# Kernel tuning notes

Measured on AMD Instinct MI355X. Metric: run time of the kernel, lower is better.

## Reference

```python
import jax, jax.numpy as jnp
import numpy as np
import math

DIM = 2048      # model dim
NH = 16         # query heads
NKV = 8         # kv heads
NREP = NH // NKV
HD = DIM // (2 * NH)   # 64: per-half head dim (q/k per head = 2*HD)
HIDDEN = 5632   # multiple_of*ceil(int(8*DIM/3)/multiple_of), multiple_of=256
EPS = 1e-5
LAMBDA = 0.8 - 0.6 * math.exp(-0.3 * 0)  # depth=0 -> 0.2
ROPE_THETA = 10000.0


def rmsnorm(x, w):
    xf = x.astype(jnp.float32)
    return (w * (xf * jax.lax.rsqrt(jnp.mean(xf * xf, axis=-1, keepdims=True) + EPS))).astype(x.dtype)


def rope(x, cos, sin):
    # x: (B, L, H, 2*HD) with interleaved (even, odd) complex pairs; cos/sin: (L, HD)
    xe, xo = x[..., 0::2], x[..., 1::2]
    c = cos[None, :, None, :]
    s = sin[None, :, None, :]
    re = xe * c - xo * s
    ro = xe * s + xo * c
    return jnp.stack([re, ro], axis=-1).reshape(x.shape)


def setup_inputs() -> dict:
    key = jax.random.key(0)
    ks = jax.random.split(key, 12)
    B, L = 1, 2048
    x = jax.random.normal(ks[0], (B, L, DIM), dtype=jnp.float32)
    # RoPE tables for per-head q/k dim 2*HD -> HD frequencies
    inv_freq = 1.0 / (ROPE_THETA ** (np.arange(0, 2 * HD, 2, dtype=np.float32) / (2 * HD)))
    t = np.arange(L, dtype=np.float32)
    ang = np.outer(t, inv_freq)  # (L, HD)
    freqs_cos = jnp.asarray(np.cos(ang), dtype=jnp.float32)
    freqs_sin = jnp.asarray(np.sin(ang), dtype=jnp.float32)
    sc = 0.02
    return {
        'x': x,
        'freqs_cos': freqs_cos,
        'freqs_sin': freqs_sin,
        'attn_norm_w': jnp.ones((DIM,), jnp.float32),
        'wq': jax.random.normal(ks[1], (DIM, DIM), jnp.float32) * sc,
        'wk': jax.random.normal(ks[2], (DIM, DIM // NREP), jnp.float32) * sc,
        'wv': jax.random.normal(ks[3], (DIM, DIM // NREP), jnp.float32) * sc,
        'wo': jax.random.normal(ks[4], (DIM, DIM), jnp.float32) * sc,
        'ffn_norm_w': jnp.ones((DIM,), jnp.float32),
        'w1': jax.random.normal(ks[5], (DIM, HIDDEN), jnp.float32) * sc,
        'w2': jax.random.normal(ks[6], (HIDDEN, DIM), jnp.float32) * sc,
        'w3': jax.random.normal(ks[7], (DIM, HIDDEN), jnp.float32) * sc,
    }


def reference(x, freqs_cos, freqs_sin, attn_norm_w, wq, wk, wv, wo, ffn_norm_w, w1, w2, w3):
    B, L, _ = x.shape
    # ---- attention branch ----
    h = rmsnorm(x, attn_norm_w)
    q = (h @ wq).reshape(B, L, NH, 2 * HD)
    k = (h @ wk).reshape(B, L, NKV, 2 * HD)
    v = (h @ wv).reshape(B, L, NKV, 2 * HD)
    q = rope(q, freqs_cos, freqs_sin)
    k = rope(k, freqs_cos, freqs_sin)
    k = jnp.repeat(k, NREP, axis=2)  # GQA expansion -> (B, L, NH, 2*HD)
    v = jnp.repeat(v, NREP, axis=2)
    q1, q2 = q[..., :HD], q[..., HD:]
    k1, k2 = k[..., :HD], k[..., HD:]
    scale = 1.0 / math.sqrt(HD)
    sc1 = jnp.einsum('bqhd,bkhd->bhqk', q1, k1) * scale
    sc2 = jnp.einsum('bqhd,bkhd->bhqk', q2, k2) * scale
    causal = jnp.tril(jnp.ones((L, L), dtype=bool))
    neg = jnp.float32(-jnp.inf)
    a1 = jax.nn.softmax(jnp.where(causal, sc1, neg), axis=-1)
    a2 = jax.nn.softmax(jnp.where(causal, sc2, neg), axis=-1)
    attn = a1 - LAMBDA * a2  # differential attention
    out = jnp.einsum('bhqk,bkhd->bqhd', attn, v).reshape(B, L, DIM)
    h2 = x + out @ wo
    # ---- SwiGLU FFN branch ----
    f = rmsnorm(h2, ffn_norm_w)
    ffn = (jax.nn.silu(f @ w1) * (f @ w3)) @ w2
    return h2 + ffn
```

## Files before the change

### kernel.cpp

```cpp
#include <hip/hip_runtime.h>
#include <hip/hip_bf16.h>

#define DIMSZ 2048
#define LSEQ 2048
#define NHEADS 16
#define NKVH 8
#define HDIM 128
#define HHALF 64
#define EPSV 1e-5f
#define LAMB 0.2f
#define SM_SCALE 0.125f

typedef __attribute__((ext_vector_type(8))) short bf16x8;
typedef __attribute__((ext_vector_type(4))) float f32x4;
typedef __hip_bfloat16 bf16;

__device__ __forceinline__ void gload_lds16(const void* g, void* l) {
    __builtin_amdgcn_global_load_lds((const __attribute__((address_space(1))) void*)g,
                                     (__attribute__((address_space(3))) void*)l, 16, 0, 0);
}

template<typename T> __device__ __forceinline__ T cvt_out(float v);
template<> __device__ __forceinline__ float cvt_out<float>(float v) { return v; }
template<> __device__ __forceinline__ bf16  cvt_out<bf16>(float v)  { return __float2bfloat16(v); }

__global__ __launch_bounds__(256) void rmsnorm_kernel(const float* __restrict__ x,
                                                      const float* __restrict__ w,
                                                      bf16* __restrict__ out)
{
    int row = blockIdx.x;
    int t = threadIdx.x;
    const float* xr = x + (size_t)row * DIMSZ;
    float4 v0 = ((const float4*)xr)[t];
    float4 v1 = ((const float4*)xr)[t + 256];
    float s = v0.x*v0.x + v0.y*v0.y + v0.z*v0.z + v0.w*v0.w
            + v1.x*v1.x + v1.y*v1.y + v1.z*v1.z + v1.w*v1.w;
    #pragma unroll
    for (int m = 1; m < 64; m <<= 1) s += __shfl_xor(s, m, 64);
    __shared__ float red[4];
    int wid = t >> 6;
    if ((t & 63) == 0) red[wid] = s;
    __syncthreads();
    float tot = red[0] + red[1] + red[2] + red[3];
    float inv = rsqrtf(tot * (1.0f / DIMSZ) + EPSV);
    float4 w0 = ((const float4*)w)[t];
    float4 w1v = ((const float4*)w)[t + 256];
    bf16* orow = out + (size_t)row * DIMSZ;
    orow[t*4 + 0] = __float2bfloat16(v0.x*inv*w0.x);
    orow[t*4 + 1] = __float2bfloat16(v0.y*inv*w0.y);
    orow[t*4 + 2] = __float2bfloat16(v0.z*inv*w0.z);
    orow[t*4 + 3] = __float2bfloat16(v0.w*inv*w0.w);
    orow[1024 + t*4 + 0] = __float2bfloat16(v1.x*inv*w1v.x);
    orow[1024 + t*4 + 1] = __float2bfloat16(v1.y*inv*w1v.y);
    orow[1024 + t*4 + 2] = __float2bfloat16(v1.z*inv*w1v.z);
    orow[1024 + t*4 + 3] = __float2bfloat16(v1.w*inv*w1v.w);
}

__global__ __launch_bounds__(256) void tcast_kernel(const float* __restrict__ in,
                                                    bf16* __restrict__ out,
                                                    int K, int N)
{
    __shared__ float tile[32][33];
    int bx = blockIdx.x, by = blockIdx.y;
    int tx = threadIdx.x & 31, tr = threadIdx.x >> 5;
    const float* src = in + (size_t)(by*32 + tr) * N + bx*32 + tx;
    #pragma unroll
    for (int r = 0; r < 32; r += 8)
        tile[tr + r][tx] = src[(size_t)r * N];
    __syncthreads();
    bf16* dst = out + (size_t)(bx*32 + tr) * K + by*32 + tx;
    #pragma unroll
    for (int r = 0; r < 32; r += 8)
        dst[(size_t)r * K] = __float2bfloat16(tile[tx][tr + r]);
}

__global__ __launch_bounds__(256) void rope_cast_kernel(const float* __restrict__ buf,
                                                        const float* __restrict__ cosT,
                                                        const float* __restrict__ sinT,
                                                        bf16* __restrict__ out,
                                                        int log2nh)
{
    int idx = blockIdx.x * 256 + threadIdx.x;
    int j = idx & 63;
    int hl = idx >> 6;
    int l = hl >> log2nh;
    float c = cosT[l * 64 + j];
    float s = sinT[l * 64 + j];
    float2 v = ((const float2*)buf)[idx];
    __hip_bfloat162 rr;
    rr.x = __float2bfloat16(v.x * c - v.y * s);
    rr.y = __float2bfloat16(v.x * s + v.y * c);
    ((__hip_bfloat162*)out)[idx] = rr;
}

template<int EPI, typename CT>
__global__ __launch_bounds__(256) void gemm_bf16(const bf16* __restrict__ A,
                                                 const bf16* __restrict__ BT,
                                                 CT* __restrict__ C,
                                                 const float* __restrict__ R,
                                                 int M, int N, int K)
{
    constexpr int BK = 32;
    __shared__ alignas(16) bf16 As[128 * BK];
    __shared__ alignas(16) bf16 Bs[128 * BK];
    int t = threadIdx.x;
    int lane = t & 63, wid = t >> 6;
    int wr = wid >> 1, wc = wid & 1;
    int row0 = blockIdx.y * 128, col0 = blockIdx.x * 128;

    f32x4 acc[4][4];
    #pragma unroll
    for (int i = 0; i < 4; ++i)
        #pragma unroll
        for (int j = 0; j < 4; ++j)
            acc[i][j] = (f32x4){0.f, 0.f, 0.f, 0.f};

    for (int k0 = 0; k0 < K; k0 += BK) {
        __syncthreads();
        #pragma unroll
        for (int s = 0; s < 2; ++s) {
            int c = s * 256 + t;
            int row = c >> 2, kc = c & 3;
            gload_lds16(A  + (size_t)(row0 + row) * K + k0 + kc * 8, (char*)As + c * 16);
            gload_lds16(BT + (size_t)(col0 + row) * K + k0 + kc * 8, (char*)Bs + c * 16);
        }
        __syncthreads();

        bf16x8 a[4], b[4];
        int ch = lane >> 4;
        #pragma unroll
        for (int i = 0; i < 4; ++i) {
            int ra = wr * 64 + i * 16 + (lane & 15);
            int rb = wc * 64 + i * 16 + (lane & 15);
            a[i] = *(const bf16x8*)((const char*)As + ra * 64 + ch * 16);
            b[i] = *(const bf16x8*)((const char*)Bs + rb * 64 + ch * 16);
        }
        #pragma unroll
        for (int i = 0; i < 4; ++i)
            #pragma unroll
            for (int j = 0; j < 4; ++j)
                acc[i][j] = __builtin_amdgcn_mfma_f32_16x16x32_bf16(a[i], b[j], acc[i][j], 0, 0, 0);
    }

    int rl = lane >> 4;
    int cl = lane & 15;
    #pragma unroll
    for (int i = 0; i < 4; ++i) {
        #pragma unroll
        for (int j = 0; j < 4; ++j) {
            #pragma unroll
            for (int r = 0; r < 4; ++r) {
                int row = row0 + wr * 64 + i * 16 + rl * 4 + r;
                int col = col0 + wc * 64 + j * 16 + cl;
                size_t idx = (size_t)row * N + col;
                float v = acc[i][j][r];
                if (EPI == 1) v += R[idx];
                else if (EPI == 2) { float uv = R[idx]; v = (uv / (1.0f + __expf(-uv))) * v; }
                C[idx] = cvt_out<CT>(v);
            }
        }
    }
}

__global__ __launch_bounds__(256) void attn_mfma_kernel(const bf16* __restrict__ Qb,
                                                        const bf16* __restrict__ Kb,
                                                        const bf16* __restrict__ Vt,
                                                        bf16* __restrict__ O)
{
    int qb = (int)gridDim.x - 1 - (int)blockIdx.x;
    int h = blockIdx.y;
    int kvh = h >> 1;
    int t = threadIdx.x;
    int lane = t & 63, w = t >> 6;
    int lr = lane & 15;
    int lk = lane >> 4;

    __shared__ alignas(16) bf16 Ksm[64 * 128];
    __shared__ alignas(16) bf16 Vsm[128 * 64];
    __shared__ alignas(16) bf16 Psm[2][64 * 64];

    bf16x8 qf[4];
    {
        const char* qrow = (const char*)Qb + ((size_t)(qb * 64 + w * 16 + lr) * (NHEADS * HDIM) + h * HDIM) * 2;
        #pragma unroll
        for (int s = 0; s < 4; ++s)
            qf[s] = *(const bf16x8*)(qrow + (s * 32 + lk * 8) * 2);
    }

    f32x4 o1[8], o2[8];
    #pragma unroll
    for (int d = 0; d < 8; ++d) { o1[d] = (f32x4){0.f,0.f,0.f,0.f}; o2[d] = (f32x4){0.f,0.f,0.f,0.f}; }
    float m1[4], l1[4], m2[4], l2[4];
    #pragma unroll
    for (int r = 0; r < 4; ++r) { m1[r] = -1e30f; m2[r] = -1e30f; l1[r] = 0.f; l2[r] = 0.f; }

    int nt = qb + 1;
    for (int it = 0; it < nt; ++it) {
        int k0 = it * 64;
        bf16x8 kreg[4], vreg[4];
        #pragma unroll
        for (int c4 = 0; c4 < 4; ++c4) {
            int c = c4 * 256 + t;
            int key = c >> 4, db = (c & 15) * 16;
            kreg[c4] = *(const bf16x8*)((const char*)Kb
                        + (size_t)(k0 + key) * (NKVH * HDIM * 2) + kvh * HDIM * 2 + db);
            int d = c >> 3, kbyte = (c & 7) * 16;
            vreg[c4] = *(const bf16x8*)((const char*)Vt
                        + ((size_t)(kvh * HDIM + d) * LSEQ + k0) * 2 + kbyte);
        }
        __syncthreads();
        #pragma unroll
        for (int c4 = 0; c4 < 4; ++c4) {
            int c = c4 * 256 + t;
            int key = c >> 4, db = (c & 15) * 16;
            *(bf16x8*)((char*)Ksm + ((key * 256 + db) ^ ((key & 7) << 4))) = kreg[c4];
            int d = c >> 3, kbyte = (c & 7) * 16;
            *(bf16x8*)((char*)Vsm + ((d * 128 + kbyte) ^ ((d & 7) << 4))) = vreg[c4];
        }
        __syncthreads();

        f32x4 s1a[4], s2a[4];
        #pragma unroll
        for (int ct = 0; ct < 4; ++ct) { s1a[ct] = (f32x4){0.f,0.f,0.f,0.f}; s2a[ct] = (f32x4){0.f,0.f,0.f,0.f}; }
        #pragma unroll
        for (int ct = 0; ct < 4; ++ct) {
            int key = ct * 16 + lr;
            int kswz = (key & 7) << 4;
            #pragma unroll
            for (int s = 0; s < 2; ++s) {
                bf16x8 kb1 = *(const bf16x8*)((const char*)Ksm + ((key * 256 + (s * 32 + lk * 8) * 2) ^ kswz));
                bf16x8 kb2 = *(const bf16x8*)((const char*)Ksm + ((key * 256 + (64 + s * 32 + lk * 8) * 2) ^ kswz));
                s1a[ct] = __builtin_amdgcn_mfma_f32_16x16x32_bf16(qf[s],     kb1, s1a[ct], 0, 0, 0);
                s2a[ct] = __builtin_amdgcn_mfma_f32_16x16x32_bf16(qf[2 + s], kb2, s2a[ct], 0, 0, 0);
            }
        }

        bool diag = (it == nt - 1);
        #pragma unroll
        for (int r = 0; r < 4; ++r) {
            int rowl = w * 16 + lk * 4 + r;
            int rg = qb * 64 + rowl;
            float v1[4], v2[4];
            #pragma unroll
            for (int ct = 0; ct < 4; ++ct) {
                v1[ct] = s1a[ct][r] * SM_SCALE;
                v2[ct] = s2a[ct][r] * SM_SCALE;
                if (diag) {
                    int cg = k0 + ct * 16 + lr;
                    if (cg > rg) { v1[ct] = -1e30f; v2[ct] = -1e30f; }
                }
            }
            float tm1 = fmaxf(fmaxf(v1[0], v1[1]), fmaxf(v1[2], v1[3]));
            float tm2 = fmaxf(fmaxf(v2[0], v2[1]), fmaxf(v2[2], v2[3]));
            #pragma unroll
            for (int msk = 1; msk < 16; msk <<= 1) {
                tm1 = fmaxf(tm1, __shfl_xor(tm1, msk, 64));
                tm2 = fmaxf(tm2, __shfl_xor(tm2, msk, 64));
            }
            float mn1 = fmaxf(m1[r], tm1), mn2 = fmaxf(m2[r], tm2);
            float ts1 = 0.f, ts2 = 0.f;
            #pragma unroll
            for (int ct = 0; ct < 4; ++ct) {
                v1[ct] = __expf(v1[ct] - mn1);
                v2[ct] = __expf(v2[ct] - mn2);
                ts1 += v1[ct]; ts2 += v2[ct];
            }
            #pragma unroll
            for (int msk = 1; msk < 16; msk <<= 1) {
                ts1 += __shfl_xor(ts1, msk, 64);
                ts2 += __shfl_xor(ts2, msk, 64);
            }
            float sc1 = __expf(m1[r] - mn1), sc2 = __expf(m2[r] - mn2);
            l1[r] = l1[r] * sc1 + ts1;
            l2[r] = l2[r] * sc2 + ts2;
            m1[r] = mn1; m2[r] = mn2;
            #pragma unroll
            for (int d = 0; d < 8; ++d) { o1[d][r] *= sc1; o2[d][r] *= sc2; }
            int pswz = ((rowl ^ (rowl >> 3)) & 7) << 4;
            #pragma unroll
            for (int ct = 0; ct < 4; ++ct) {
                int byte0 = (rowl * 128 + (ct * 16 + lr) * 2) ^ pswz;
                *(bf16*)((char*)Psm[0] + byte0) = __float2bfloat16(v1[ct]);
                *(bf16*)((char*)Psm[1] + byte0) = __float2bfloat16(v2[ct]);
            }
        }
        asm volatile("s_waitcnt lgkmcnt(0)" ::: "memory");
        __builtin_amdgcn_sched_barrier(0);

        int prow = w * 16 + lr;
        int pswz2 = ((prow ^ (prow >> 3)) & 7) << 4;
        bf16x8 p1f[2], p2f[2];
        #pragma unroll
        for (int s = 0; s < 2; ++s) {
            int pb = (prow * 128 + (s * 32 + lk * 8) * 2) ^ pswz2;
            p1f[s] = *(const bf16x8*)((const char*)Psm[0] + pb);
            p2f[s] = *(const bf16x8*)((const char*)Psm[1] + pb);
        }
        #pragma unroll
        for (int dt = 0; dt < 8; ++dt) {
            int d = dt * 16 + lr;
            int vswz = (d & 7) << 4;
            #pragma unroll
            for (int s = 0; s < 2; ++s) {
                bf16x8 vf = *(const bf16x8*)((const char*)Vsm + ((d * 128 + (s * 32 + lk * 8) * 2) ^ vswz));
                o1[dt] = __builtin_amdgcn_mfma_f32_16x16x32_bf16(p1f[s], vf, o1[dt], 0, 0, 0);
                o2[dt] = __builtin_amdgcn_mfma_f32_16x16x32_bf16(p2f[s], vf, o2[dt], 0, 0, 0);
            }
        }
    }

    #pragma unroll
    for (int r = 0; r < 4; ++r) {
        float inv1 = 1.0f / l1[r];
        float inv2 = LAMB / l2[r];
        bf16* dst = O + (size_t)(qb * 64 + w * 16 + lk * 4 + r) * DIMSZ + h * HDIM;
        #pragma unroll
        for (int dt = 0; dt < 8; ++dt)
            dst[dt * 16 + lr] = __float2bfloat16(o1[dt][r] * inv1 - o2[dt][r] * inv2);
    }
}

extern "C" void kernel_launch(void* const* d_in, const int* in_sizes, int n_in,
                              void* d_out, int out_size, void* d_ws, size_t ws_size,
                              hipStream_t stream)
{
    const float* x      = (const float*)d_in[0];
    const float* fcos   = (const float*)d_in[1];
    const float* fsin   = (const float*)d_in[2];
    const float* attn_w = (const float*)d_in[3];
    const float* wq     = (const float*)d_in[4];
    const float* wk     = (const float*)d_in[5];
    const float* wv     = (const float*)d_in[6];
    const float* wo     = (const float*)d_in[7];
    const float* ffn_w  = (const float*)d_in[8];
    const float* w1     = (const float*)d_in[9];
    const float* w2     = (const float*)d_in[10];
    const float* w3     = (const float*)d_in[11];
    float* out = (float*)d_out;
    char*  wsb = (char*)d_ws;

    bf16*  h    = (bf16*) (wsb + 0);
    float* q    = (float*)(wsb + (size_t)( 8u << 20));
    float* kb   = (float*)(wsb + (size_t)(24u << 20));
    float* vb   = (float*)(wsb + (size_t)(32u << 20));
    bf16*  q_bf = (bf16*) (wsb + 0);
    bf16*  k_bf = (bf16*) (wsb + (size_t)( 8u << 20));
    bf16*  vt   = (bf16*) (wsb + (size_t)(12u << 20));
    bf16*  att  = (bf16*) (wsb + (size_t)(40u << 20));
    float* u    = (float*)(wsb + 0);
    bf16*  f    = (bf16*) (wsb + (size_t)(48u << 20));
    bf16*  g    = (bf16*) (wsb + (size_t)(56u << 20));
    bf16*  W    = (bf16*) (wsb + (size_t)(80u << 20));

    dim3 blk(256);

    rmsnorm_kernel<<<LSEQ, blk, 0, stream>>>(x, attn_w, h);

    tcast_kernel<<<dim3(64, 64), blk, 0, stream>>>(wq, W, 2048, 2048);
    gemm_bf16<0, float><<<dim3(16, 16), blk, 0, stream>>>(h, W, q, nullptr, 2048, 2048, 2048);
    tcast_kernel<<<dim3(32, 64), blk, 0, stream>>>(wk, W, 2048, 1024);
    gemm_bf16<0, float><<<dim3(8, 16), blk, 0, stream>>>(h, W, kb, nullptr, 2048, 1024, 2048);
    tcast_kernel<<<dim3(32, 64), blk, 0, stream>>>(wv, W, 2048, 1024);
    gemm_bf16<0, float><<<dim3(8, 16), blk, 0, stream>>>(h, W, vb, nullptr, 2048, 1024, 2048);

    rope_cast_kernel<<<(LSEQ * NHEADS * 64) / 256, blk, 0, stream>>>(q, fcos, fsin, q_bf, 4);
    rope_cast_kernel<<<(LSEQ * NKVH * 64) / 256, blk, 0, stream>>>(kb, fcos, fsin, k_bf, 3);
    tcast_kernel<<<dim3(32, 64), blk, 0, stream>>>(vb, vt, 2048, 1024);

    attn_mfma_kernel<<<dim3(LSEQ / 64, NHEADS), blk, 0, stream>>>(q_bf, k_bf, vt, att);

    tcast_kernel<<<dim3(64, 64), blk, 0, stream>>>(wo, W, 2048, 2048);
    gemm_bf16<1, float><<<dim3(16, 16), blk, 0, stream>>>(att, W, out, x, 2048, 2048, 2048);

    rmsnorm_kernel<<<LSEQ, blk, 0, stream>>>(out, ffn_w, f);

    tcast_kernel<<<dim3(176, 64), blk, 0, stream>>>(w1, W, 2048, 5632);
    gemm_bf16<0, float><<<dim3(44, 16), blk, 0, stream>>>(f, W, u, nullptr, 2048, 5632, 2048);
    tcast_kernel<<<dim3(176, 64), blk, 0, stream>>>(w3, W, 2048, 5632);
    gemm_bf16<2, bf16><<<dim3(44, 16), blk, 0, stream>>>(f, W, g, u, 2048, 5632, 2048);
    tcast_kernel<<<dim3(64, 176), blk, 0, stream>>>(w2, W, 5632, 2048);
    gemm_bf16<1, float><<<dim3(16, 16), blk, 0, stream>>>(g, W, out, out, 2048, 2048, 5632);
}
```

Before: 938.0 us.

## Fuse QKV and W1/W3 GEMMs, split-K the Wo and W2 projections

Result: faster. 781.6 us (-16.7%).

```diff
diff --git a/kernel.cpp b/kernel.cpp
--- a/kernel.cpp
+++ b/kernel.cpp
@@ -18,6 +18,11 @@
 __device__ __forceinline__ void gload_lds16(const void* g, void* l) {
     __builtin_amdgcn_global_load_lds((const __attribute__((address_space(1))) void*)g,
                                      (__attribute__((address_space(3))) void*)l, 16, 0, 0);
+}
+
+__device__ __forceinline__ float bf2f(short s) {
+    unsigned u = ((unsigned)(unsigned short)s) << 16;
+    return __builtin_bit_cast(float, u);
 }
 
 template<typename T> __device__ __forceinline__ T cvt_out(float v);
@@ -58,15 +63,15 @@
 
 __global__ __launch_bounds__(256) void tcast_kernel(const float* __restrict__ in,
                                                     bf16* __restrict__ out,
-                                                    int K, int N)
+                                                    int K, int N, int inStride)
 {
     __shared__ float tile[32][33];
     int bx = blockIdx.x, by = blockIdx.y;
     int tx = threadIdx.x & 31, tr = threadIdx.x >> 5;
-    const float* src = in + (size_t)(by*32 + tr) * N + bx*32 + tx;
+    const float* src = in + (size_t)(by*32 + tr) * inStride + bx*32 + tx;
     #pragma unroll
     for (int r = 0; r < 32; r += 8)
-        tile[tr + r][tx] = src[(size_t)r * N];
+        tile[tr + r][tx] = src[(size_t)r * inStride];
     __syncthreads();
     bf16* dst = out + (size_t)(bx*32 + tr) * K + by*32 + tx;
     #pragma unroll
@@ -74,7 +79,8 @@
         dst[(size_t)r * K] = __float2bfloat16(tile[tx][tr + r]);
 }
 
-__global__ __launch_bounds__(256) void rope_cast_kernel(const float* __restrict__ buf,
+__global__ __launch_bounds__(256) void rope_cast_kernel(const float* __restrict__ src,
+                                                        int srcStrideF2, int srcOffF2,
                                                         const float* __restrict__ cosT,
                                                         const float* __restrict__ sinT,
                                                         bf16* __restrict__ out,
@@ -82,22 +88,21 @@
 {
     int idx = blockIdx.x * 256 + threadIdx.x;
     int j = idx & 63;
-    int hl = idx >> 6;
-    int l = hl >> log2nh;
+    int l = idx >> (6 + log2nh);
+    int rem = idx & ((64 << log2nh) - 1);
     float c = cosT[l * 64 + j];
     float s = sinT[l * 64 + j];
-    float2 v = ((const float2*)buf)[idx];
+    float2 v = ((const float2*)src)[(size_t)l * srcStrideF2 + srcOffF2 + rem];
     __hip_bfloat162 rr;
     rr.x = __float2bfloat16(v.x * c - v.y * s);
     rr.y = __float2bfloat16(v.x * s + v.y * c);
     ((__hip_bfloat162*)out)[idx] = rr;
 }
 
-template<int EPI, typename CT>
+template<typename CT, bool SPLIT>
 __global__ __launch_bounds__(256) void gemm_bf16(const bf16* __restrict__ A,
                                                  const bf16* __restrict__ BT,
                                                  CT* __restrict__ C,
-                                                 const float* __restrict__ R,
                                                  int M, int N, int K)
 {
     constexpr int BK = 32;
@@ -108,6 +113,14 @@
     int wr = wid >> 1, wc = wid & 1;
     int row0 = blockIdx.y * 128, col0 = blockIdx.x * 128;
 
+    int kBeg = 0, kEnd = K;
+    if (SPLIT) {
+        int kh = K / (int)gridDim.z;
+        kBeg = blockIdx.z * kh;
+        kEnd = kBeg + kh;
+        C += (size_t)blockIdx.z * M * N;
+    }
+
     f32x4 acc[4][4];
     #pragma unroll
     for (int i = 0; i < 4; ++i)
@@ -115,7 +128,7 @@
         for (int j = 0; j < 4; ++j)
             acc[i][j] = (f32x4){0.f, 0.f, 0.f, 0.f};
 
-    for (int k0 = 0; k0 < K; k0 += BK) {
+    for (int k0 = kBeg; k0 < kEnd; k0 += BK) {
         __syncthreads();
         #pragma unroll
         for (int s = 0; s < 2; ++s) {
@@ -152,14 +165,39 @@
             for (int r = 0; r < 4; ++r) {
                 int row = row0 + wr * 64 + i * 16 + rl * 4 + r;
                 int col = col0 + wc * 64 + j * 16 + cl;
-                size_t idx = (size_t)row * N + col;
-                float v = acc[i][j][r];
-                if (EPI == 1) v += R[idx];
-                else if (EPI == 2) { float uv = R[idx]; v = (uv / (1.0f + __expf(-uv))) * v; }
-                C[idx] = cvt_out<CT>(v);
-            }
-        }
-    }
+                C[(size_t)row * N + col] = cvt_out<CT>(acc[i][j][r]);
+            }
+        }
+    }
+}
+
+__global__ __launch_bounds__(256) void combine_kernel(float* __restrict__ out,
+                                                      const float* __restrict__ p0,
+                                                      const float* __restrict__ p1,
+                                                      const float* __restrict__ r)
+{
+    int i = blockIdx.x * 256 + threadIdx.x;
+    float4 a = ((const float4*)p0)[i];
+    float4 b = ((const float4*)p1)[i];
+    float4 c = ((const float4*)r)[i];
+    float4 o = {a.x + b.x + c.x, a.y + b.y + c.y, a.z + b.z + c.z, a.w + b.w + c.w};
+    ((float4*)out)[i] = o;
+}
+
+__global__ __launch_bounds__(256) void silu_mul_kernel(const bf16* __restrict__ u,
+                                                       bf16* __restrict__ g)
+{
+    int idx = blockIdx.x * 256 + threadIdx.x;
+    int row = idx / 704, c8 = (idx % 704) * 8;
+    bf16x8 a = *(const bf16x8*)(u + (size_t)row * 11264 + c8);
+    bf16x8 b = *(const bf16x8*)(u + (size_t)row * 11264 + 5632 + c8);
+    alignas(16) bf16 o[8];
+    #pragma unroll
+    for (int j = 0; j < 8; ++j) {
+        float fa = bf2f(a[j]), fb = bf2f(b[j]);
+        o[j] = __float2bfloat16((fa / (1.0f + __expf(-fa))) * fb);
+    }
+    *(bf16x8*)(g + (size_t)row * 5632 + c8) = *(bf16x8*)o;
 }
 
 __global__ __launch_bounds__(256) void attn_mfma_kernel(const bf16* __restrict__ Qb,
@@ -340,44 +378,47 @@
     char*  wsb = (char*)d_ws;
 
     bf16*  h    = (bf16*) (wsb + 0);
-    float* q    = (float*)(wsb + (size_t)( 8u << 20));
-    float* kb   = (float*)(wsb + (size_t)(24u << 20));
-    float* vb   = (float*)(wsb + (size_t)(32u << 20));
-    bf16*  q_bf = (bf16*) (wsb + 0);
-    bf16*  k_bf = (bf16*) (wsb + (size_t)( 8u << 20));
-    bf16*  vt   = (bf16*) (wsb + (size_t)(12u << 20));
-    bf16*  att  = (bf16*) (wsb + (size_t)(40u << 20));
-    float* u    = (float*)(wsb + 0);
-    bf16*  f    = (bf16*) (wsb + (size_t)(48u << 20));
-    bf16*  g    = (bf16*) (wsb + (size_t)(56u << 20));
-    bf16*  W    = (bf16*) (wsb + (size_t)(80u << 20));
-
+    bf16*  W4   = (bf16*) (wsb + (size_t)(16u << 20));
+    float* qkv  = (float*)(wsb + (size_t)(40u << 20));
+    bf16*  q_bf = (bf16*) (wsb + (size_t)(80u << 20));
+    bf16*  k_bf = (bf16*) (wsb + (size_t)(88u << 20));
+    bf16*  vt   = (bf16*) (wsb + (size_t)(92u << 20));
+    bf16*  att  = (bf16*) (wsb + 0);
+    bf16*  WoT  = (bf16*) (wsb + (size_t)(16u << 20));
+    float* Pw   = (float*)(wsb + (size_t)(40u << 20));
+    bf16*  f    = (bf16*) (wsb + 0);
+    bf16*  Wbig = (bf16*) (wsb + (size_t)( 8u << 20));
+    bf16*  u13  = (bf16*) (wsb + (size_t)(52u << 20));
+    bf16*  g    = (bf16*) (wsb + (size_t)( 8u << 20));
+    bf16*  W2T  = (bf16*) (wsb + (size_t)(30u << 20));
+    float* P2   = (float*)(wsb + (size_t)(52u << 20));
+
+    const size_t PSZ = (size_t)2048 * 2048;
     dim3 blk(256);
 
     rmsnorm_kernel<<<LSEQ, blk, 0, stream>>>(x, attn_w, h);
-
-    tcast_kernel<<<dim3(64, 64), blk, 0, stream>>>(wq, W, 2048, 2048);
-    gemm_bf16<0, float><<<dim3(16, 16), blk, 0, stream>>>(h, W, q, nullptr, 2048, 2048, 2048);
-    tcast_kernel<<<dim3(32, 64), blk, 0, stream>>>(wk, W, 2048, 1024);
-    gemm_bf16<0, float><<<dim3(8, 16), blk, 0, stream>>>(h, W, kb, nullptr, 2048, 1024, 2048);
-    tcast_kernel<<<dim3(32, 64), blk, 0, stream>>>(wv, W, 2048, 1024);
-    gemm_bf16<0, float><<<dim3(8, 16), blk, 0, stream>>>(h, W, vb, nullptr, 2048, 1024, 2048);
-
-    rope_cast_kernel<<<(LSEQ * NHEADS * 64) / 256, blk, 0, stream>>>(q, fcos, fsin, q_bf, 4);
-    rope_cast_kernel<<<(LSEQ * NKVH * 64) / 256, blk, 0, stream>>>(kb, fcos, fsin, k_bf, 3);
-    tcast_kernel<<<dim3(32, 64), blk, 0, stream>>>(vb, vt, 2048, 1024);
+    tcast_kernel<<<dim3(64, 64), blk, 0, stream>>>(wq, W4,                 2048, 2048, 2048);
+    tcast_kernel<<<dim3(32, 64), blk, 0, stream>>>(wk, W4 + 2048*2048,     2048, 1024, 1024);
+    tcast_kernel<<<dim3(32, 64), blk, 0, stream>>>(wv, W4 + 3072*2048,     2048, 1024, 1024);
+    gemm_bf16<float, false><<<dim3(32, 16), blk, 0, stream>>>(h, W4, qkv, 2048, 4096, 2048);
+
+    rope_cast_kernel<<<8192, blk, 0, stream>>>(qkv, 2048,    0, fcos, fsin, q_bf, 4);
+    rope_cast_kernel<<<4096, blk, 0, stream>>>(qkv, 2048, 1024, fcos, fsin, k_bf, 3);
+    tcast_kernel<<<dim3(32, 64), blk, 0, stream>>>(qkv + 3072, vt, 2048, 1024, 4096);
 
     attn_mfma_kernel<<<dim3(LSEQ / 64, NHEADS), blk, 0, stream>>>(q_bf, k_bf, vt, att);
 
-    tcast_kernel<<<dim3(64, 64), blk, 0, stream>>>(wo, W, 2048, 2048);
-    gemm_bf16<1, float><<<dim3(16, 16), blk, 0, stream>>>(att, W, out, x, 2048, 2048, 2048);
+    tcast_kernel<<<dim3(64, 64), blk, 0, stream>>>(wo, WoT, 2048, 2048, 2048);
+    gemm_bf16<float, true><<<dim3(16, 16, 2), blk, 0, stream>>>(att, WoT, Pw, 2048, 2048, 2048);
+    combine_kernel<<<4096, blk, 0, stream>>>(out, Pw, Pw + PSZ, x);
 
     rmsnorm_kernel<<<LSEQ, blk, 0, stream>>>(out, ffn_w, f);
-
-    tcast_kernel<<<dim3(176, 64), blk, 0, stream>>>(w1, W, 2048, 5632);
-    gemm_bf16<0, float><<<dim3(44, 16), blk, 0, stream>>>(f, W, u, nullptr, 2048, 5632, 2048);
-    tcast_kernel<<<dim3(176, 64), blk, 0, stream>>>(w3, W, 2048, 5632);
-    gemm_bf16<2, bf16><<<dim3(44, 16), blk, 0, stream>>>(f, W, g, u, 2048, 5632, 2048);
-    tcast_kernel<<<dim3(64, 176), blk, 0, stream>>>(w2, W, 5632, 2048);
-    gemm_bf16<1, float><<<dim3(16, 16), blk, 0, stream>>>(g, W, out, out, 2048, 2048, 5632);
-}
+    tcast_kernel<<<dim3(176, 64), blk, 0, stream>>>(w1, Wbig,             2048, 5632, 5632);
+    tcast_kernel<<<dim3(176, 64), blk, 0, stream>>>(w3, Wbig + 5632*2048, 2048, 5632, 5632);
+    gemm_bf16<bf16, false><<<dim3(88, 16), blk, 0, stream>>>(f, Wbig, u13, 2048, 11264, 2048);
+    silu_mul_kernel<<<5632, blk, 0, stream>>>(u13, g);
+
+    tcast_kernel<<<dim3(64, 176), blk, 0, stream>>>(w2, W2T, 5632, 2048, 2048);
+    gemm_bf16<float, true><<<dim3(16, 16, 2), blk, 0, stream>>>(g, W2T, P2, 2048, 2048, 5632);
+    combine_kernel<<<4096, blk, 0, stream>>>(out, P2, P2 + PSZ, out);
+}
```
